# Optimization experiments

Measured on AMD Instinct MI355X. Metric: run time of the kernel, lower is better.

Reference implementation:

```python
import jax, jax.numpy as jnp
import numpy as np

# Dimensions
N = 12288      # fact nodes (batched graph)
B = 64         # examples in batch
R = 36         # image regions per example (hardcoded .repeat(36,1) in source)
E = 196608     # fact-graph edges (avg degree 16)
D_IN = 512     # in_dims
D_OUT = 512    # out_dims
P = 256        # img_att_proj_dim
D_IMG = 1024   # img_dim


def setup_inputs() -> dict:
    key = jax.random.key(0)
    ks = jax.random.split(key, 12)

    def w(k, shape, fan_in):
        return jax.random.normal(k, shape, dtype=jnp.float32) / np.float32(np.sqrt(fan_in))

    return {
        "h": jax.random.normal(ks[0], (N, D_IN), dtype=jnp.float32),
        "img_feats": jax.random.normal(ks[1], (B, R, D_IMG), dtype=jnp.float32),
        "batch_ids": jax.random.randint(ks[2], (N,), 0, B, dtype=jnp.int32),
        "src": jax.random.randint(ks[3], (E,), 0, N, dtype=jnp.int32),
        "dst": jax.random.randint(ks[4], (E,), 0, N, dtype=jnp.int32),
        # cross_att_fact_proj
        "Wf": w(ks[5], (D_IN, P), D_IN), "bf": jnp.zeros((P,), jnp.float32),
        # cross_att_img_proj
        "Wi": w(ks[6], (D_IMG, P), D_IMG), "bi": jnp.zeros((P,), jnp.float32),
        # att_proj (P -> 1)
        "Wa": w(ks[7], (P, 1), P), "ba": jnp.zeros((1,), jnp.float32),
        # node_fc
        "Wn": w(ks[8], (D_IN, D_OUT), D_IN), "bn": jnp.zeros((D_OUT,), jnp.float32),
        # img_fc
        "Wim": w(ks[9], (D_IMG, D_OUT), D_IMG), "bim": jnp.zeros((D_OUT,), jnp.float32),
        # apply_fc (2*out -> out)
        "Wap": w(ks[10], (2 * D_OUT, D_OUT), 2 * D_OUT), "bap": jnp.zeros((D_OUT,), jnp.float32),
    }


def reference(h, img_feats, batch_ids, src, dst,
              Wf, bf, Wi, bi, Wa, ba, Wn, bn, Wim, bim, Wap, bap):
    # ---- apply_node: cross-modal attention over the node's 36 image regions ----
    node_proj = h @ Wf + bf                                   # [N, P]
    img_proj = img_feats @ Wi + bi                            # [B, R, P]
    img_proj_n = img_proj[batch_ids]                          # [N, R, P] gather per node's example
    logits = (jnp.tanh(node_proj[:, None, :] + img_proj_n) @ Wa)[..., 0] + ba[0]  # [N, R]
    att = jax.nn.softmax(logits, axis=1)                      # softmax over 36 regions
    img_n = img_feats[batch_ids]                              # [N, R, D_IMG]
    img = jnp.einsum("nr,nrd->nd", att, img_n)               # [N, D_IMG] attended image feature
    h1 = h @ Wn + bn                                          # node_fc updates 'h' [N, D_OUT]

    # ---- update_all: copy_src('h') messages, sum reduce over in-neighbors ----
    neigh = jax.ops.segment_sum(h1[src], dst, num_segments=N)  # [N, D_OUT]
    msg = neigh + img @ Wim + bim                              # [N, D_OUT]

    # ---- reduce: concat + apply_fc + relu ----
    out = jax.nn.relu(jnp.concatenate([msg, h1], axis=1) @ Wap + bap)  # [N, D_OUT]
    return out
```

## Files before the change

### kernel.cpp

```cpp
#include <hip/hip_runtime.h>
#include <cstdint>
#include <cstddef>

#define N_NODES 12288
#define B_EX    64
#define R_REG   36
#define E_EDGES 196608
#define DD_IN   512
#define DD_OUT  512
#define P_DIM   256
#define D_IMG   1024
#define TANH_C  2.885390081777927f

#define A2_LD     1024
#define NEIGH_OFF 0
#define H1_OFF    512

typedef unsigned short ushort;
typedef __bf16 bf16x8 __attribute__((ext_vector_type(8)));
typedef float f32x4 __attribute__((ext_vector_type(4)));
typedef ushort ushort4v __attribute__((ext_vector_type(4)));
typedef ushort ushort8v __attribute__((ext_vector_type(8)));

__device__ __forceinline__ ushort f2bf(float f) {
    uint32_t u = __float_as_uint(f);
    uint32_t r = (u + 0x7fffu + ((u >> 16) & 1u)) >> 16;
    return (ushort)r;
}
__device__ __forceinline__ float bf2f(ushort u) {
    return __uint_as_float(((uint32_t)u) << 16);
}
__device__ __forceinline__ void gload_lds16(const void* g, void* l) {
    __builtin_amdgcn_global_load_lds((const __attribute__((address_space(1))) void*)g,
                                     (__attribute__((address_space(3))) void*)l, 16, 0, 0);
}
__device__ __forceinline__ void stage_f32(const float* __restrict__ src, void* ldsDst) {
    float4 v0 = *(const float4*)src;
    float4 v1 = *(const float4*)(src + 4);
    ushort8v o;
    o[0] = f2bf(v0.x); o[1] = f2bf(v0.y); o[2] = f2bf(v0.z); o[3] = f2bf(v0.w);
    o[4] = f2bf(v1.x); o[5] = f2bf(v1.y); o[6] = f2bf(v1.z); o[7] = f2bf(v1.w);
    *(ushort8v*)ldsDst = o;
}
__device__ __forceinline__ float fexp2(float x) {
    float r; asm("v_exp_f32 %0, %1" : "=v"(r) : "v"(x)); return r;
}
__device__ __forceinline__ float frcp(float x) {
    float r; asm("v_rcp_f32 %0, %1" : "=v"(r) : "v"(x)); return r;
}
__device__ __forceinline__ int xcd_swz(int lin, int nwg) {
    if ((nwg & 7) == 0) return (lin & 7) * (nwg >> 3) + (lin >> 3);
    return lin;
}

#define PCVT_BLKS (N_NODES * DD_IN / 4 / 256)
#define TR_BLKS   352
#define ZERO_INTS (2 * N_NODES + 2 * B_EX)
#define ZERO_BLKS ((ZERO_INTS + 255) / 256)
__global__ __launch_bounds__(256) void preamble(
    const float* __restrict__ h, ushort* __restrict__ h_bf,
    const float* __restrict__ Wf, const float* __restrict__ Wn,
    const float* __restrict__ Wi, const float* __restrict__ Wap,
    ushort* __restrict__ WfnT, ushort* __restrict__ WiZT,
    ushort* __restrict__ Wap1T, ushort* __restrict__ BT2,
    int* __restrict__ zero_p)
{
    if (blockIdx.x < PCVT_BLKS) {
        int i = blockIdx.x * 256 + threadIdx.x;
        float4 v = ((const float4*)h)[i];
        ushort4v o;
        o[0] = f2bf(v.x); o[1] = f2bf(v.y); o[2] = f2bf(v.z); o[3] = f2bf(v.w);
        ((ushort4v*)h_bf)[i] = o;
        return;
    }
    if (blockIdx.x >= PCVT_BLKS + TR_BLKS) {
        int i = (blockIdx.x - PCVT_BLKS - TR_BLKS) * 256 + threadIdx.x;
        if (i < ZERO_INTS) zero_p[i] = 0;
        return;
    }
    int t = blockIdx.x - PCVT_BLKS;
    const float* W; ushort* WT; int N, ldt, gx;
    if (t < 32)       { W = Wf;  WT = WfnT;                        N = 256; ldt = 512;  gx = 4; }
    else if (t < 96)  { W = Wn;  WT = WfnT + 256 * 512;            N = 512; ldt = 512;  gx = 8; t -= 32; }
    else if (t < 160) { W = Wi;  WT = WiZT;                        N = 256; ldt = 1024; gx = 4; t -= 96; }
    else if (t < 224) { W = Wap; WT = Wap1T;                       N = 512; ldt = 512;  gx = 8; t -= 160; }
    else if (t < 288) { W = Wap; WT = BT2 + NEIGH_OFF;             N = 512; ldt = 1024; gx = 8; t -= 224; }
    else              { W = Wap + 512 * 512; WT = BT2 + H1_OFF;    N = 512; ldt = 1024; gx = 8; t -= 288; }
    const int n0 = (t % gx) * 64, k0 = (t / gx) * 64;

    __shared__ float tt[64][65];
    const int tx = threadIdx.x & 15, ty = threadIdx.x >> 4;
#pragma unroll
    for (int r = 0; r < 4; ++r) {
        float4 v = *(const float4*)&W[(size_t)(k0 + ty * 4 + r) * N + n0 + tx * 4];
        tt[ty * 4 + r][tx * 4 + 0] = v.x;
        tt[ty * 4 + r][tx * 4 + 1] = v.y;
        tt[ty * 4 + r][tx * 4 + 2] = v.z;
        tt[ty * 4 + r][tx * 4 + 3] = v.w;
    }
    __syncthreads();
    const int nl = threadIdx.x >> 2, kq = (threadIdx.x & 3) * 16;
    ushort u[16] __attribute__((aligned(16)));
#pragma unroll
    for (int c = 0; c < 16; ++c) u[c] = f2bf(tt[kq + c][nl]);
    ushort* d = &WT[(size_t)(n0 + nl) * ldt + k0 + kq];
    *(ushort8v*)d = *(ushort8v*)&u[0];
    *(ushort8v*)(d + 8) = *(ushort8v*)&u[8];
}

#define CNT_BLKS (E_EDGES / 256 + N_NODES / 256)
__global__ __launch_bounds__(256) void k2_count_wp(
    const int* __restrict__ dst, const int* __restrict__ bid,
    int* __restrict__ deg, int* __restrict__ bcnt,
    const ushort* __restrict__ Wap1T, const float* __restrict__ Wim,
    ushort* __restrict__ WiZT)
{
    __shared__ ushort As[128 * 64];
    __shared__ ushort Bs[128 * 64];
    if (blockIdx.x < CNT_BLKS) {
        int b = blockIdx.x;
        if (b < E_EDGES / 256) {
            atomicAdd(&deg[dst[b * 256 + threadIdx.x]], 1);
        } else {
            atomicAdd(&bcnt[bid[(b - E_EDGES / 256) * 256 + threadIdx.x]], 1);
        }
        return;
    }
    const int K = DD_IN;
    const int tid = threadIdx.x;
    const int lane = tid & 63;
    const int wid = tid >> 6;
    const int wm = wid >> 1, wn = wid & 1;
    const int lin = blockIdx.x - CNT_BLKS;
    const int m0 = (lin >> 3) * 128, n0 = (lin & 7) * 128;

    f32x4 acc[4][4] = {};
    const int srow = tid >> 3;
    const int schk = tid & 7;
    const char* AsB = (const char*)As;
    const char* BsB = (const char*)Bs;

    for (int k0 = 0; k0 < K; k0 += 64) {
#pragma unroll
        for (int i = 0; i < 4; ++i) {
            int row = i * 32 + srow;
            int ca = (schk ^ (row & 7)) * 8;
            gload_lds16(Wap1T + (size_t)(m0 + row) * K + k0 + ca,
                        (char*)As + i * 4096 + wid * 1024);
            stage_f32(Wim + (size_t)(n0 + row) * K + k0 + ca,
                      (char*)Bs + i * 4096 + wid * 1024 + lane * 16);
        }
        __syncthreads();
#pragma unroll
        for (int kk = 0; kk < 2; ++kk) {
            const int kc = kk * 4 + (lane >> 4);
            bf16x8 af[4], bfr[4];
#pragma unroll
            for (int i = 0; i < 4; ++i) {
                int row = wm * 64 + i * 16 + (lane & 15);
                af[i] = *(const bf16x8*)(AsB + row * 128 + ((kc ^ (row & 7)) << 4));
            }
#pragma unroll
            for (int j = 0; j < 4; ++j) {
                int col = wn * 64 + j * 16 + (lane & 15);
                bfr[j] = *(const bf16x8*)(BsB + col * 128 + ((kc ^ (col & 7)) << 4));
            }
#pragma unroll
            for (int i = 0; i < 4; ++i)
#pragma unroll
                for (int j = 0; j < 4; ++j)
                    acc[i][j] = __builtin_amdgcn_mfma_f32_16x16x32_bf16(af[i], bfr[j], acc[i][j], 0, 0, 0);
        }
        __syncthreads();
    }

#pragma unroll
    for (int i = 0; i < 4; ++i)
#pragma unroll
        for (int j = 0; j < 4; ++j)
#pragma unroll
            for (int q = 0; q < 4; ++q) {
                int row = m0 + wm * 64 + i * 16 + (lane >> 4) * 4 + q;
                int col = n0 + wn * 64 + j * 16 + (lane & 15);
                WiZT[(size_t)(256 + row) * D_IMG + col] = f2bf(acc[i][j][q]);
            }
}

__global__ __launch_bounds__(256) void k3_scan_imgz(
    const int* __restrict__ deg, int* __restrict__ offs,
    const int* __restrict__ bcnt, int* __restrict__ boffs,
    const float* __restrict__ bim, const float* __restrict__ Wap,
    const float* __restrict__ bap, float* __restrict__ bp,
    const float* __restrict__ imgf, const ushort* __restrict__ WiZT,
    const float* __restrict__ bi, float* __restrict__ img_proj,
    ushort* __restrict__ Z)
{
    __shared__ ushort As[128 * 64];
    __shared__ ushort Bs[128 * 64];
    const int t = threadIdx.x;
    if (blockIdx.x < 4) {
        if (blockIdx.x == 0) {
            __shared__ int s[257];
            const int base = t * 48;
            int sum = 0;
            for (int j = 0; j < 48; ++j) sum += deg[base + j];
            s[t] = sum;
            __syncthreads();
            if (t == 0) {
                int acc = 0;
                for (int i = 0; i < 256; ++i) { int v = s[i]; s[i] = acc; acc += v; }
                s[256] = acc;
            }
            __syncthreads();
            int run = s[t];
            for (int j = 0; j < 48; ++j) { offs[base + j] = run; run += deg[base + j]; }
            if (t == 255) offs[N_NODES] = s[256];
        } else if (blockIdx.x == 1) {
            if (t == 0) {
                int acc = 0;
                for (int i = 0; i < B_EX; ++i) { boffs[i] = acc; acc += bcnt[i]; }
                boffs[B_EX] = acc;
            }
        } else {
            int n = (blockIdx.x - 2) * 256 + t;
            float s = bap[n];
            for (int k = 0; k < DD_OUT; ++k) s += bim[k] * Wap[(size_t)k * DD_OUT + n];
            bp[n] = s;
        }
        return;
    }
    const int K = D_IMG;
    const int lane = t & 63;
    const int wid = t >> 6;
    const int wm = wid >> 1, wn = wid & 1;
    const int lin = blockIdx.x - 4;
    const int m0 = (lin / 6) * 128, n0 = (lin % 6) * 128;

    f32x4 acc[4][4] = {};
    const int srow = t >> 3;
    const int schk = t & 7;
    const char* AsB = (const char*)As;
    const char* BsB = (const char*)Bs;

    for (int k0 = 0; k0 < K; k0 += 64) {
#pragma unroll
        for (int i = 0; i < 4; ++i) {
            int row = i * 32 + srow;
            int ca = (schk ^ (row & 7)) * 8;
            stage_f32(imgf + (size_t)(m0 + row) * K + k0 + ca,
                      (char*)As + i * 4096 + wid * 1024 + lane * 16);
            gload_lds16(WiZT + (size_t)(n0 + row) * K + k0 + ca,
                        (char*)Bs + i * 4096 + wid * 1024);
        }
        __syncthreads();
#pragma unroll
        for (int kk = 0; kk < 2; ++kk) {
            const int kc = kk * 4 + (lane >> 4);
            bf16x8 af[4], bfr[4];
#pragma unroll
            for (int i = 0; i < 4; ++i) {
                int row = wm * 64 + i * 16 + (lane & 15);
                af[i] = *(const bf16x8*)(AsB + row * 128 + ((kc ^ (row & 7)) << 4));
            }
#pragma unroll
            for (int j = 0; j < 4; ++j) {
                int col = wn * 64 + j * 16 + (lane & 15);
                bfr[j] = *(const bf16x8*)(BsB + col * 128 + ((kc ^ (col & 7)) << 4));
            }
#pragma unroll
            for (int i = 0; i < 4; ++i)
#pragma unroll
                for (int j = 0; j < 4; ++j)
                    acc[i][j] = __builtin_amdgcn_mfma_f32_16x16x32_bf16(af[i], bfr[j], acc[i][j], 0, 0, 0);
        }
        __syncthreads();
    }

    if (n0 < 256) {
#pragma unroll
        for (int i = 0; i < 4; ++i)
#pragma unroll
            for (int j = 0; j < 4; ++j)
#pragma unroll
                for (int q = 0; q < 4; ++q) {
                    int row = m0 + wm * 64 + i * 16 + (lane >> 4) * 4 + q;
                    int col = n0 + wn * 64 + j * 16 + (lane & 15);
                    img_proj[(size_t)row * P_DIM + col] = acc[i][j][q] + bi[col];
                }
    } else {
#pragma unroll
        for (int i = 0; i < 4; ++i)
#pragma unroll
            for (int j = 0; j < 4; ++j)
#pragma unroll
                for (int q = 0; q < 4; ++q) {
                    int row = m0 + wm * 64 + i * 16 + (lane >> 4) * 4 + q;
                    int col = n0 - 256 + wn * 64 + j * 16 + (lane & 15);
                    Z[(size_t)row * DD_OUT + col] = f2bf(acc[i][j][q]);
                }
    }
}

__global__ __launch_bounds__(256) void k4_scatter_ff(
    const int* __restrict__ src, const int* __restrict__ dst,
    const int* __restrict__ offs, int* __restrict__ cur, int* __restrict__ ssrc,
    const int* __restrict__ bid, const int* __restrict__ boffs,
    int* __restrict__ bcur, int* __restrict__ nlist,
    const ushort* __restrict__ h_bf, const ushort* __restrict__ WfnT,
    const float* __restrict__ biasF, const float* __restrict__ biasN,
    float* __restrict__ node_proj_s, ushort* __restrict__ A2)
{
    __shared__ ushort As[128 * 64];
    __shared__ ushort Bs[64 * 64];
    if (blockIdx.x < CNT_BLKS) {
        int b = blockIdx.x;
        if (b < E_EDGES / 256) {
            int i = b * 256 + threadIdx.x;
            int d = dst[i];
            int p = offs[d] + atomicAdd(&cur[d], 1);
            ssrc[p] = src[i];
        } else {
            int i = (b - E_EDGES / 256) * 256 + threadIdx.x;
            int e = bid[i];
            int p = boffs[e] + atomicAdd(&bcur[e], 1);
            nlist[p] = i;
        }
        return;
    }
    const int K = DD_IN;
    const int tid = threadIdx.x;
    const int lane = tid & 63;
    const int wid = tid >> 6;
    const int lin = xcd_swz(blockIdx.x - CNT_BLKS, 1152);
    const int m0 = (lin / 12) * 128, n0 = (lin % 12) * 64;

    f32x4 acc[2][4] = {};
    const int srow = tid >> 3;
    const int schk = tid & 7;
    const char* AsB = (const char*)As;
    const char* BsB = (const char*)Bs;

    for (int k0 = 0; k0 < K; k0 += 64) {
#pragma unroll
        for (int i = 0; i < 4; ++i) {
            int row = i * 32 + srow;
            int ca = (schk ^ (row & 7)) * 8;
            gload_lds16(h_bf + (size_t)(m0 + row) * K + k0 + ca,
                        (char*)As + i * 4096 + wid * 1024);
        }
#pragma unroll
        for (int i = 0; i < 2; ++i) {
            int row = i * 32 + srow;
            int cb = (schk ^ (row & 7)) * 8;
            gload_lds16(WfnT + (size_t)(n0 + row) * K + k0 + cb,
                        (char*)Bs + i * 4096 + wid * 1024);
        }
        __syncthreads();
#pragma unroll
        for (int kk = 0; kk < 2; ++kk) {
            const int kc = kk * 4 + (lane >> 4);
            bf16x8 af[2], bfr[4];
#pragma unroll
            for (int i = 0; i < 2; ++i) {
                int row = wid * 32 + i * 16 + (lane & 15);
                af[i] = *(const bf16x8*)(AsB + row * 128 + ((kc ^ (row & 7)) << 4));
            }
#pragma unroll
            for (int j = 0; j < 4; ++j) {
                int col = j * 16 + (lane & 15);
                bfr[j] = *(const bf16x8*)(BsB + col * 128 + ((kc ^ (col & 7)) << 4));
            }
#pragma unroll
            for (int i = 0; i < 2; ++i)
#pragma unroll
                for (int j = 0; j < 4; ++j)
                    acc[i][j] = __builtin_amdgcn_mfma_f32_16x16x32_bf16(af[i], bfr[j], acc[i][j], 0, 0, 0);
        }
        __syncthreads();
    }

    if (n0 < 256) {
#pragma unroll
        for (int i = 0; i < 2; ++i)
#pragma unroll
            for (int j = 0; j < 4; ++j)
#pragma unroll
                for (int q = 0; q < 4; ++q) {
                    int row = m0 + wid * 32 + i * 16 + (lane >> 4) * 4 + q;
                    int col = n0 + j * 16 + (lane & 15);
                    node_proj_s[(size_t)row * P_DIM + col] = (acc[i][j][q] + biasF[col]) * TANH_C;
                }
    } else {
#pragma unroll
        for (int i = 0; i < 2; ++i)
#pragma unroll
            for (int j = 0; j < 4; ++j)
#pragma unroll
                for (int q = 0; q < 4; ++q) {
                    int row = m0 + wid * 32 + i * 16 + (lane >> 4) * 4 + q;
                    int col = n0 - 256 + j * 16 + (lane & 15);
                    A2[(size_t)row * A2_LD + H1_OFF + col] = f2bf(acc[i][j][q] + biasN[col]);
                }
    }
}

__device__ __forceinline__ void acc8(float* a, uint4 v) {
    a[0] += bf2f((ushort)(v.x & 0xffffu)); a[1] += bf2f((ushort)(v.x >> 16));
    a[2] += bf2f((ushort)(v.y & 0xffffu)); a[3] += bf2f((ushort)(v.y >> 16));
    a[4] += bf2f((ushort)(v.z & 0xffffu)); a[5] += bf2f((ushort)(v.z >> 16));
    a[6] += bf2f((ushort)(v.w & 0xffffu)); a[7] += bf2f((ushort)(v.w >> 16));
}

__global__ __launch_bounds__(256) void k5_att_gather(
    const float* __restrict__ node_proj_s, const float* __restrict__ img_proj,
    const int* __restrict__ batch_ids, const float* __restrict__ Wa,
    const ushort* __restrict__ Z, ushort* __restrict__ imgz,
    const int* __restrict__ off, const int* __restrict__ ssrc,
    const ushort* __restrict__ A2h1, ushort* __restrict__ A2nb)
{
    __shared__ float red[4][R_REG][20];
    const int lane = threadIdx.x & 63;
    const int wv = threadIdx.x >> 6;
    if (blockIdx.x < N_NODES / 4) {
        const int n = blockIdx.x * 4 + wv;
        const int b = batch_ids[n];

        const float4 nps = *(const float4*)(node_proj_s + (size_t)n * P_DIM + 4 * lane);
        const float4 wa = *(const float4*)(Wa + 4 * lane);
        const float* ip0 = img_proj + (size_t)b * R_REG * P_DIM + 4 * lane;

#pragma unroll
        for (int r = 0; r < R_REG; ++r) {
            float4 ip = *(const float4*)(ip0 + (size_t)r * P_DIM);
            float t0 = fexp2(fmaf(ip.x, TANH_C, nps.x));
            float t1 = fexp2(fmaf(ip.y, TANH_C, nps.y));
            float t2 = fexp2(fmaf(ip.z, TANH_C, nps.z));
            float t3 = fexp2(fmaf(ip.w, TANH_C, nps.w));
            float p;
            p = wa.x * frcp(t0 + 1.f);
            p = fmaf(wa.y, frcp(t1 + 1.f), p);
            p = fmaf(wa.z, frcp(t2 + 1.f), p);
            p = fmaf(wa.w, frcp(t3 + 1.f), p);
            p += __shfl_xor(p, 16);
            p += __shfl_xor(p, 32);
            if (lane < 16) red[wv][r][lane] = p;
        }
        __syncthreads();

        float logit = -INFINITY;
        if (lane < R_REG) {
            const float* row = &red[wv][lane][0];
            float4 a = *(const float4*)row;
            float4 bq = *(const float4*)(row + 4);
            float4 c = *(const float4*)(row + 8);
            float4 d = *(const float4*)(row + 12);
            float s01 = ((a.x + a.y) + (a.z + a.w)) + ((bq.x + bq.y) + (bq.z + bq.w));
            float s23 = ((c.x + c.y) + (c.z + c.w)) + ((d.x + d.y) + (d.z + d.w));
            logit = -2.f * (s01 + s23);
        }
        float m = logit;
#pragma unroll
        for (int o = 32; o; o >>= 1) m = fmaxf(m, __shfl_xor(m, o));
        float e = (lane < R_REG) ? __expf(logit - m) : 0.f;
        float s = e;
#pragma unroll
        for (int o = 32; o; o >>= 1) s += __shfl_xor(s, o);
        float inv_s = frcp(s);
        if (lane < R_REG) red[wv][lane][16] = e * inv_s;

        float az[8] = {};
        const ushort* zb = Z + (size_t)b * R_REG * DD_OUT + lane * 8;
#pragma unroll 4
        for (int r = 0; r < R_REG; ++r) {
            uint4 zv = *(const uint4*)(zb + (size_t)r * DD_OUT);
            float a = red[wv][r][16];
            az[0] = fmaf(a, bf2f((ushort)(zv.x & 0xffffu)), az[0]);
            az[1] = fmaf(a, bf2f((ushort)(zv.x >> 16)),     az[1]);
            az[2] = fmaf(a, bf2f((ushort)(zv.y & 0xffffu)), az[2]);
            az[3] = fmaf(a, bf2f((ushort)(zv.y >> 16)),     az[3]);
            az[4] = fmaf(a, bf2f((ushort)(zv.z & 0xffffu)), az[4]);
            az[5] = fmaf(a, bf2f((ushort)(zv.z >> 16)),     az[5]);
            az[6] = fmaf(a, bf2f((ushort)(zv.w & 0xffffu)), az[6]);
            az[7] = fmaf(a, bf2f((ushort)(zv.w >> 16)),     az[7]);
        }
        ushort8v zo;
#pragma unroll
        for (int i = 0; i < 8; ++i) zo[i] = f2bf(az[i]);
        *(ushort8v*)(imgz + (size_t)n * DD_OUT + lane * 8) = zo;
        return;
    }
    const int n = (blockIdx.x - N_NODES / 4) * 4 + wv;
    const int e0 = off[n], e1 = off[n + 1];

    float a[8] = {};
    int e = e0;
    for (; e + 4 <= e1; e += 4) {
        int s0 = ssrc[e], s1 = ssrc[e + 1], s2 = ssrc[e + 2], s3 = ssrc[e + 3];
        uint4 v0 = *(const uint4*)(A2h1 + (size_t)s0 * A2_LD + lane * 8);
        uint4 v1 = *(const uint4*)(A2h1 + (size_t)s1 * A2_LD + lane * 8);
        uint4 v2 = *(const uint4*)(A2h1 + (size_t)s2 * A2_LD + lane * 8);
        uint4 v3 = *(const uint4*)(A2h1 + (size_t)s3 * A2_LD + lane * 8);
        acc8(a, v0); acc8(a, v1); acc8(a, v2); acc8(a, v3);
    }
    for (; e < e1; ++e) {
        int s0 = ssrc[e];
        uint4 v0 = *(const uint4*)(A2h1 + (size_t)s0 * A2_LD + lane * 8);
        acc8(a, v0);
    }
    ushort8v o;
#pragma unroll
    for (int i = 0; i < 8; ++i) o[i] = f2bf(a[i]);
    *(ushort8v*)(A2nb + (size_t)n * A2_LD + lane * 8) = o;
}

__global__ __launch_bounds__(256) void gemm_out(
    const ushort* __restrict__ A, const ushort* __restrict__ BT,
    const float* __restrict__ bias, const ushort* __restrict__ Cadd,
    float* __restrict__ Cf)
{
    __shared__ ushort As[128 * 64];
    __shared__ ushort Bs[64 * 64];
    const int K = A2_LD;
    const int tid = threadIdx.x;
    const int lane = tid & 63;
    const int wid = tid >> 6;
    const int lin = xcd_swz(blockIdx.y * 8 + blockIdx.x, 768);
    const int m0 = (lin >> 3) * 128, n0 = (lin & 7) * 64;

    f32x4 acc[2][4] = {};
    const int srow = tid >> 3;
    const int schk = tid & 7;
    const char* AsB = (const char*)As;
    const char* BsB = (const char*)Bs;

    for (int k0 = 0; k0 < K; k0 += 64) {
#pragma unroll
        for (int i = 0; i < 4; ++i) {
            int row = i * 32 + srow;
            int ca = (schk ^ (row & 7)) * 8;
            gload_lds16(A + (size_t)(m0 + row) * K + k0 + ca,
                        (char*)As + i * 4096 + wid * 1024);
        }
#pragma unroll
        for (int i = 0; i < 2; ++i) {
            int row = i * 32 + srow;
            int cb = (schk ^ (row & 7)) * 8;
            gload_lds16(BT + (size_t)(n0 + row) * K + k0 + cb,
                        (char*)Bs + i * 4096 + wid * 1024);
        }
        __syncthreads();
#pragma unroll
        for (int kk = 0; kk < 2; ++kk) {
            const int kc = kk * 4 + (lane >> 4);
            bf16x8 af[2], bfr[4];
#pragma unroll
            for (int i = 0; i < 2; ++i) {
                int row = wid * 32 + i * 16 + (lane & 15);
                af[i] = *(const bf16x8*)(AsB + row * 128 + ((kc ^ (row & 7)) << 4));
            }
#pragma unroll
            for (int j = 0; j < 4; ++j) {
                int col = j * 16 + (lane & 15);
                bfr[j] = *(const bf16x8*)(BsB + col * 128 + ((kc ^ (col & 7)) << 4));
            }
#pragma unroll
            for (int i = 0; i < 2; ++i)
#pragma unroll
                for (int j = 0; j < 4; ++j)
                    acc[i][j] = __builtin_amdgcn_mfma_f32_16x16x32_bf16(af[i], bfr[j], acc[i][j], 0, 0, 0);
        }
        __syncthreads();
    }

#pragma unroll
    for (int i = 0; i < 2; ++i)
#pragma unroll
        for (int j = 0; j < 4; ++j)
#pragma unroll
            for (int q = 0; q < 4; ++q) {
                int row = m0 + wid * 32 + i * 16 + (lane >> 4) * 4 + q;
                int col = n0 + j * 16 + (lane & 15);
                float v = acc[i][j][q] + bias[col] + bf2f(Cadd[(size_t)row * DD_OUT + col]);
                Cf[(size_t)row * DD_OUT + col] = fmaxf(v, 0.f);
            }
}

extern "C" void kernel_launch(void* const* d_in, const int* in_sizes, int n_in,
                              void* d_out, int out_size, void* d_ws, size_t ws_size,
                              hipStream_t stream) {
    const float* h         = (const float*)d_in[0];
    const float* img_feats = (const float*)d_in[1];
    const int*   batch_ids = (const int*)d_in[2];
    const int*   src       = (const int*)d_in[3];
    const int*   dst       = (const int*)d_in[4];
    const float* Wf  = (const float*)d_in[5];
    const float* bf  = (const float*)d_in[6];
    const float* Wi  = (const float*)d_in[7];
    const float* bi  = (const float*)d_in[8];
    const float* Wa  = (const float*)d_in[9];
    const float* Wn  = (const float*)d_in[11];
    const float* bn  = (const float*)d_in[12];
    const float* Wim = (const float*)d_in[13];
    const float* bim = (const float*)d_in[14];
    const float* Wap = (const float*)d_in[15];
    const float* bap = (const float*)d_in[16];
    float* out = (float*)d_out;
    float* ws  = (float*)d_ws;

    ushort* A2      = (ushort*)(ws + 0);
    ushort* imgz    = (ushort*)(ws + 6291456);
    float*  node_proj = ws + 12582912;
    float*  img_proj  = ws + 15728640;
    ushort* Z      = (ushort*)(ws + 16760832);
    ushort* h_bf   = (ushort*)(ws + 17350656);
    ushort* WfnT   = (ushort*)(ws + 20496384);
    ushort* WiZT   = (ushort*)(ws + 20692992);
    ushort* Wap1T  = (ushort*)(ws + 21086208);
    ushort* BT2    = (ushort*)(ws + 21217280);
    float*  bprime = ws + 21479424;
    int* deg  = (int*)(ws + 21479936);
    int* cur  = deg + N_NODES;
    int* bcnt = cur + N_NODES;
    int* bcur = bcnt + B_EX;
    int* offs = bcur + B_EX;
    int* boffs = offs + N_NODES + 1;
    int* ssrc = boffs + B_EX + 1;
    int* nlist = ssrc + E_EDGES;

    dim3 blk(256);

    preamble<<<dim3(PCVT_BLKS + TR_BLKS + ZERO_BLKS), blk, 0, stream>>>(
        h, h_bf, Wf, Wn, Wi, Wap, WfnT, WiZT, Wap1T, BT2, deg);
    k2_count_wp<<<dim3(CNT_BLKS + 32), blk, 0, stream>>>(
        dst, batch_ids, deg, bcnt, Wap1T, Wim, WiZT);
    k3_scan_imgz<<<dim3(4 + 108), blk, 0, stream>>>(
        deg, offs, bcnt, boffs, bim, Wap, bap, bprime,
        img_feats, WiZT, bi, img_proj, Z);
    k4_scatter_ff<<<dim3(CNT_BLKS + 1152), blk, 0, stream>>>(
        src, dst, offs, cur, ssrc, batch_ids, boffs, bcur, nlist,
        h_bf, WfnT, bf, bn, node_proj, A2);
    k5_att_gather<<<dim3(2 * (N_NODES / 4)), blk, 0, stream>>>(
        node_proj, img_proj, batch_ids, Wa, Z, imgz,
        offs, ssrc, A2 + H1_OFF, A2 + NEIGH_OFF);
    gemm_out<<<dim3(8, 96), blk, 0, stream>>>(A2, BT2, bprime, imgz, out);
}
```

Measured before the change: 209.9 us.

## Re-partition kernel stages: merge node-feature GEMM with imgZ GEMM, batch-sort in one block

Moves the per-example node counting and sort into a single block of the count kernel, which uses shared-memory atomics and removes the bcnt/boffs global arrays. The node_fc/fact-projection GEMM moves into the same launch as the image projection GEMM. The attention computation now runs alongside the edge scatter, iterating nodes in batch-sorted order so that nodes sharing an example's image data run close together. The goal is better overlap between stages and cache reuse of img_proj and Z. The trade-off is a serial single-block sort of 12288 nodes and a different load balance across the merged kernels.

```diff
diff --git a/kernel.cpp b/kernel.cpp
--- a/kernel.cpp
+++ b/kernel.cpp
@@ -55,8 +55,8 @@
 
 #define PCVT_BLKS (N_NODES * DD_IN / 4 / 256)
 #define TR_BLKS   352
-#define ZERO_INTS (2 * N_NODES + 2 * B_EX)
-#define ZERO_BLKS ((ZERO_INTS + 255) / 256)
+#define ZERO_INTS (2 * N_NODES)
+#define ZERO_BLKS (ZERO_INTS / 256)
 __global__ __launch_bounds__(256) void preamble(
     const float* __restrict__ h, ushort* __restrict__ h_bf,
     const float* __restrict__ Wf, const float* __restrict__ Wn,
@@ -108,21 +108,38 @@
     *(ushort8v*)(d + 8) = *(ushort8v*)&u[8];
 }
 
-#define CNT_BLKS (E_EDGES / 256 + N_NODES / 256)
-__global__ __launch_bounds__(256) void k2_count_wp(
+#define ECNT_BLKS (E_EDGES / 256)
+__global__ __launch_bounds__(256) void k2_count_sort_wp(
     const int* __restrict__ dst, const int* __restrict__ bid,
-    int* __restrict__ deg, int* __restrict__ bcnt,
+    int* __restrict__ deg, int* __restrict__ nlist,
     const ushort* __restrict__ Wap1T, const float* __restrict__ Wim,
     ushort* __restrict__ WiZT)
 {
     __shared__ ushort As[128 * 64];
     __shared__ ushort Bs[128 * 64];
-    if (blockIdx.x < CNT_BLKS) {
-        int b = blockIdx.x;
-        if (b < E_EDGES / 256) {
-            atomicAdd(&deg[dst[b * 256 + threadIdx.x]], 1);
-        } else {
-            atomicAdd(&bcnt[bid[(b - E_EDGES / 256) * 256 + threadIdx.x]], 1);
+    if (blockIdx.x < ECNT_BLKS) {
+        atomicAdd(&deg[dst[blockIdx.x * 256 + threadIdx.x]], 1);
+        return;
+    }
+    if (blockIdx.x == ECNT_BLKS) {
+        __shared__ int bc[B_EX];
+        __shared__ int bo[B_EX];
+        if (threadIdx.x < B_EX) bc[threadIdx.x] = 0;
+        __syncthreads();
+        for (int i = threadIdx.x; i < N_NODES; i += 256)
+            atomicAdd(&bc[bid[i]], 1);
+        __syncthreads();
+        if (threadIdx.x == 0) {
+            int acc = 0;
+            for (int i = 0; i < B_EX; ++i) { bo[i] = acc; acc += bc[i]; }
+        }
+        __syncthreads();
+        if (threadIdx.x < B_EX) bc[threadIdx.x] = 0;
+        __syncthreads();
+        for (int i = threadIdx.x; i < N_NODES; i += 256) {
+            int b = bid[i];
+            int p = bo[b] + atomicAdd(&bc[b], 1);
+            nlist[p] = i;
         }
         return;
     }
@@ -131,7 +148,7 @@
     const int lane = tid & 63;
     const int wid = tid >> 6;
     const int wm = wid >> 1, wn = wid & 1;
-    const int lin = blockIdx.x - CNT_BLKS;
+    const int lin = blockIdx.x - (ECNT_BLKS + 1);
     const int m0 = (lin >> 3) * 128, n0 = (lin & 7) * 128;
 
     f32x4 acc[4][4] = {};
@@ -186,19 +203,23 @@
             }
 }
 
-__global__ __launch_bounds__(256) void k3_scan_imgz(
+#define IMGZ_BASE 3
+#define FF_BASE   111
+__global__ __launch_bounds__(256) void k3_scan_imgz_ff(
     const int* __restrict__ deg, int* __restrict__ offs,
-    const int* __restrict__ bcnt, int* __restrict__ boffs,
     const float* __restrict__ bim, const float* __restrict__ Wap,
     const float* __restrict__ bap, float* __restrict__ bp,
     const float* __restrict__ imgf, const ushort* __restrict__ WiZT,
     const float* __restrict__ bi, float* __restrict__ img_proj,
-    ushort* __restrict__ Z)
+    ushort* __restrict__ Z,
+    const ushort* __restrict__ h_bf, const ushort* __restrict__ WfnT,
+    const float* __restrict__ biasF, const float* __restrict__ biasN,
+    float* __restrict__ node_proj_s, ushort* __restrict__ A2)
 {
     __shared__ ushort As[128 * 64];
     __shared__ ushort Bs[128 * 64];
     const int t = threadIdx.x;
-    if (blockIdx.x < 4) {
+    if (blockIdx.x < IMGZ_BASE) {
         if (blockIdx.x == 0) {
             __shared__ int s[257];
             const int base = t * 48;
@@ -215,128 +236,94 @@
             int run = s[t];
             for (int j = 0; j < 48; ++j) { offs[base + j] = run; run += deg[base + j]; }
             if (t == 255) offs[N_NODES] = s[256];
-        } else if (blockIdx.x == 1) {
-            if (t == 0) {
-                int acc = 0;
-                for (int i = 0; i < B_EX; ++i) { boffs[i] = acc; acc += bcnt[i]; }
-                boffs[B_EX] = acc;
-            }
         } else {
-            int n = (blockIdx.x - 2) * 256 + t;
+            int n = (blockIdx.x - 1) * 256 + t;
             float s = bap[n];
             for (int k = 0; k < DD_OUT; ++k) s += bim[k] * Wap[(size_t)k * DD_OUT + n];
             bp[n] = s;
         }
         return;
     }
-    const int K = D_IMG;
     const int lane = t & 63;
     const int wid = t >> 6;
-    const int wm = wid >> 1, wn = wid & 1;
-    const int lin = blockIdx.x - 4;
-    const int m0 = (lin / 6) * 128, n0 = (lin % 6) * 128;
-
-    f32x4 acc[4][4] = {};
+    if (blockIdx.x < FF_BASE) {
+        const int K = D_IMG;
+        const int wm = wid >> 1, wn = wid & 1;
+        const int lin = blockIdx.x - IMGZ_BASE;
+        const int m0 = (lin / 6) * 128, n0 = (lin % 6) * 128;
+
+        f32x4 acc[4][4] = {};
+        const int srow = t >> 3;
+        const int schk = t & 7;
+        const char* AsB = (const char*)As;
+        const char* BsB = (const char*)Bs;
+
+        for (int k0 = 0; k0 < K; k0 += 64) {
+#pragma unroll
+            for (int i = 0; i < 4; ++i) {
+                int row = i * 32 + srow;
+                int ca = (schk ^ (row & 7)) * 8;
+                stage_f32(imgf + (size_t)(m0 + row) * K + k0 + ca,
+                          (char*)As + i * 4096 + wid * 1024 + lane * 16);
+                gload_lds16(WiZT + (size_t)(n0 + row) * K + k0 + ca,
+                            (char*)Bs + i * 4096 + wid * 1024);
+            }
+            __syncthreads();
+#pragma unroll
+            for (int kk = 0; kk < 2; ++kk) {
+                const int kc = kk * 4 + (lane >> 4);
+                bf16x8 af[4], bfr[4];
+#pragma unroll
+                for (int i = 0; i < 4; ++i) {
+                    int row = wm * 64 + i * 16 + (lane & 15);
+                    af[i] = *(const bf16x8*)(AsB + row * 128 + ((kc ^ (row & 7)) << 4));
+                }
+#pragma unroll
+                for (int j = 0; j < 4; ++j) {
+                    int col = wn * 64 + j * 16 + (lane & 15);
+                    bfr[j] = *(const bf16x8*)(BsB + col * 128 + ((kc ^ (col & 7)) << 4));
+                }
+#pragma unroll
+                for (int i = 0; i < 4; ++i)
+#pragma unroll
+                    for (int j = 0; j < 4; ++j)
+                        acc[i][j] = __builtin_amdgcn_mfma_f32_16x16x32_bf16(af[i], bfr[j], acc[i][j], 0, 0, 0);
+            }
+            __syncthreads();
+        }
+
+        if (n0 < 256) {
+#pragma unroll
+            for (int i = 0; i < 4; ++i)
+#pragma unroll
+                for (int j = 0; j < 4; ++j)
+#pragma unroll
+                    for (int q = 0; q < 4; ++q) {
+                        int row = m0 + wm * 64 + i * 16 + (lane >> 4) * 4 + q;
+                        int col = n0 + wn * 64 + j * 16 + (lane & 15);
+                        img_proj[(size_t)row * P_DIM + col] = acc[i][j][q] + bi[col];
+                    }
+        } else {
+#pragma unroll
+            for (int i = 0; i < 4; ++i)
+#pragma unroll
+                for (int j = 0; j < 4; ++j)
+#pragma unroll
+                    for (int q = 0; q < 4; ++q) {
+                        int row = m0 + wm * 64 + i * 16 + (lane >> 4) * 4 + q;
+                        int col = n0 - 256 + wn * 64 + j * 16 + (lane & 15);
+                        Z[(size_t)row * DD_OUT + col] = f2bf(acc[i][j][q]);
+                    }
+        }
+        return;
+    }
+    const int K = DD_IN;
+    const int lin = xcd_swz(blockIdx.x - FF_BASE, 1152);
+    const int m0 = (lin / 12) * 128, n0 = (lin % 12) * 64;
+
+    f32x4 acc[2][4] = {};
     const int srow = t >> 3;
     const int schk = t & 7;
-    const char* AsB = (const char*)As;
-    const char* BsB = (const char*)Bs;
-
-    for (int k0 = 0; k0 < K; k0 += 64) {
-#pragma unroll
-        for (int i = 0; i < 4; ++i) {
-            int row = i * 32 + srow;
-            int ca = (schk ^ (row & 7)) * 8;
-            stage_f32(imgf + (size_t)(m0 + row) * K + k0 + ca,
-                      (char*)As + i * 4096 + wid * 1024 + lane * 16);
-            gload_lds16(WiZT + (size_t)(n0 + row) * K + k0 + ca,
-                        (char*)Bs + i * 4096 + wid * 1024);
-        }
-        __syncthreads();
-#pragma unroll
-        for (int kk = 0; kk < 2; ++kk) {
-            const int kc = kk * 4 + (lane >> 4);
-            bf16x8 af[4], bfr[4];
-#pragma unroll
-            for (int i = 0; i < 4; ++i) {
-                int row = wm * 64 + i * 16 + (lane & 15);
-                af[i] = *(const bf16x8*)(AsB + row * 128 + ((kc ^ (row & 7)) << 4));
-            }
-#pragma unroll
-            for (int j = 0; j < 4; ++j) {
-                int col = wn * 64 + j * 16 + (lane & 15);
-                bfr[j] = *(const bf16x8*)(BsB + col * 128 + ((kc ^ (col & 7)) << 4));
-            }
-#pragma unroll
-            for (int i = 0; i < 4; ++i)
-#pragma unroll
-                for (int j = 0; j < 4; ++j)
-                    acc[i][j] = __builtin_amdgcn_mfma_f32_16x16x32_bf16(af[i], bfr[j], acc[i][j], 0, 0, 0);
-        }
-        __syncthreads();
-    }
-
-    if (n0 < 256) {
-#pragma unroll
-        for (int i = 0; i < 4; ++i)
-#pragma unroll
-            for (int j = 0; j < 4; ++j)
-#pragma unroll
-                for (int q = 0; q < 4; ++q) {
-                    int row = m0 + wm * 64 + i * 16 + (lane >> 4) * 4 + q;
-                    int col = n0 + wn * 64 + j * 16 + (lane & 15);
-                    img_proj[(size_t)row * P_DIM + col] = acc[i][j][q] + bi[col];
-                }
-    } else {
-#pragma unroll
-        for (int i = 0; i < 4; ++i)
-#pragma unroll
-            for (int j = 0; j < 4; ++j)
-#pragma unroll
-                for (int q = 0; q < 4; ++q) {
-                    int row = m0 + wm * 64 + i * 16 + (lane >> 4) * 4 + q;
-                    int col = n0 - 256 + wn * 64 + j * 16 + (lane & 15);
-                    Z[(size_t)row * DD_OUT + col] = f2bf(acc[i][j][q]);
-                }
-    }
-}
-
-__global__ __launch_bounds__(256) void k4_scatter_ff(
-    const int* __restrict__ src, const int* __restrict__ dst,
-    const int* __restrict__ offs, int* __restrict__ cur, int* __restrict__ ssrc,
-    const int* __restrict__ bid, const int* __restrict__ boffs,
-    int* __restrict__ bcur, int* __restrict__ nlist,
-    const ushort* __restrict__ h_bf, const ushort* __restrict__ WfnT,
-    const float* __restrict__ biasF, const float* __restrict__ biasN,
-    float* __restrict__ node_proj_s, ushort* __restrict__ A2)
-{
-    __shared__ ushort As[128 * 64];
-    __shared__ ushort Bs[64 * 64];
-    if (blockIdx.x < CNT_BLKS) {
-        int b = blockIdx.x;
-        if (b < E_EDGES / 256) {
-            int i = b * 256 + threadIdx.x;
-            int d = dst[i];
-            int p = offs[d] + atomicAdd(&cur[d], 1);
-            ssrc[p] = src[i];
-        } else {
-            int i = (b - E_EDGES / 256) * 256 + threadIdx.x;
-            int e = bid[i];
-            int p = boffs[e] + atomicAdd(&bcur[e], 1);
-            nlist[p] = i;
-        }
-        return;
-    }
-    const int K = DD_IN;
-    const int tid = threadIdx.x;
-    const int lane = tid & 63;
-    const int wid = tid >> 6;
-    const int lin = xcd_swz(blockIdx.x - CNT_BLKS, 1152);
-    const int m0 = (lin / 12) * 128, n0 = (lin % 12) * 64;
-
-    f32x4 acc[2][4] = {};
-    const int srow = tid >> 3;
-    const int schk = tid & 7;
     const char* AsB = (const char*)As;
     const char* BsB = (const char*)Bs;
 
@@ -404,6 +391,91 @@
     }
 }
 
+__global__ __launch_bounds__(256) void k4_scatter_att(
+    const int* __restrict__ src, const int* __restrict__ dst,
+    const int* __restrict__ offs, int* __restrict__ cur, int* __restrict__ ssrc,
+    const float* __restrict__ node_proj_s, const float* __restrict__ img_proj,
+    const int* __restrict__ batch_ids, const float* __restrict__ Wa,
+    const ushort* __restrict__ Z, ushort* __restrict__ imgz,
+    const int* __restrict__ nlist)
+{
+    __shared__ float red[4][R_REG][20];
+    if (blockIdx.x < ECNT_BLKS) {
+        int i = blockIdx.x * 256 + threadIdx.x;
+        int d = dst[i];
+        int p = offs[d] + atomicAdd(&cur[d], 1);
+        ssrc[p] = src[i];
+        return;
+    }
+    const int lane = threadIdx.x & 63;
+    const int wv = threadIdx.x >> 6;
+    const int n = nlist[(blockIdx.x - ECNT_BLKS) * 4 + wv];
+    const int b = batch_ids[n];
+
+    const float4 nps = *(const float4*)(node_proj_s + (size_t)n * P_DIM + 4 * lane);
+    const float4 wa = *(const float4*)(Wa + 4 * lane);
+    const float* ip0 = img_proj + (size_t)b * R_REG * P_DIM + 4 * lane;
+
+#pragma unroll
+    for (int r = 0; r < R_REG; ++r) {
+        float4 ip = *(const float4*)(ip0 + (size_t)r * P_DIM);
+        float t0 = fexp2(fmaf(ip.x, TANH_C, nps.x));
+        float t1 = fexp2(fmaf(ip.y, TANH_C, nps.y));
+        float t2 = fexp2(fmaf(ip.z, TANH_C, nps.z));
+        float t3 = fexp2(fmaf(ip.w, TANH_C, nps.w));
+        float p;
+        p = wa.x * frcp(t0 + 1.f);
+        p = fmaf(wa.y, frcp(t1 + 1.f), p);
+        p = fmaf(wa.z, frcp(t2 + 1.f), p);
+        p = fmaf(wa.w, frcp(t3 + 1.f), p);
+        p += __shfl_xor(p, 16);
+        p += __shfl_xor(p, 32);
+        if (lane < 16) red[wv][r][lane] = p;
+    }
+    __syncthreads();
+
+    float logit = -INFINITY;
+    if (lane < R_REG) {
+        const float* row = &red[wv][lane][0];
+        float4 a = *(const float4*)row;
+        float4 bq = *(const float4*)(row + 4);
+        float4 c = *(const float4*)(row + 8);
+        float4 d = *(const float4*)(row + 12);
+        float s01 = ((a.x + a.y) + (a.z + a.w)) + ((bq.x + bq.y) + (bq.z + bq.w));
+        float s23 = ((c.x + c.y) + (c.z + c.w)) + ((d.x + d.y) + (d.z + d.w));
+        logit = -2.f * (s01 + s23);
+    }
+    float m = logit;
+#pragma unroll
+    for (int o = 32; o; o >>= 1) m = fmaxf(m, __shfl_xor(m, o));
+    float e = (lane < R_REG) ? __expf(logit - m) : 0.f;
+    float s = e;
+#pragma unroll
+    for (int o = 32; o; o >>= 1) s += __shfl_xor(s, o);
+    float inv_s = frcp(s);
+    if (lane < R_REG) red[wv][lane][16] = e * inv_s;
+
+    float az[8] = {};
+    const ushort* zb = Z + (size_t)b * R_REG * DD_OUT + lane * 8;
+#pragma unroll 4
+    for (int r = 0; r < R_REG; ++r) {
+        uint4 zv = *(const uint4*)(zb + (size_t)r * DD_OUT);
+        float a = red[wv][r][16];
+        az[0] = fmaf(a, bf2f((ushort)(zv.x & 0xffffu)), az[0]);
+        az[1] = fmaf(a, bf2f((ushort)(zv.x >> 16)),     az[1]);
+        az[2] = fmaf(a, bf2f((ushort)(zv.y & 0xffffu)), az[2]);
+        az[3] = fmaf(a, bf2f((ushort)(zv.y >> 16)),     az[3]);
+        az[4] = fmaf(a, bf2f((ushort)(zv.z & 0xffffu)), az[4]);
+        az[5] = fmaf(a, bf2f((ushort)(zv.z >> 16)),     az[5]);
+        az[6] = fmaf(a, bf2f((ushort)(zv.w & 0xffffu)), az[6]);
+        az[7] = fmaf(a, bf2f((ushort)(zv.w >> 16)),     az[7]);
+    }
+    ushort8v zo;
+#pragma unroll
+    for (int i = 0; i < 8; ++i) zo[i] = f2bf(az[i]);
+    *(ushort8v*)(imgz + (size_t)n * DD_OUT + lane * 8) = zo;
+}
+
 __device__ __forceinline__ void acc8(float* a, uint4 v) {
     a[0] += bf2f((ushort)(v.x & 0xffffu)); a[1] += bf2f((ushort)(v.x >> 16));
     a[2] += bf2f((ushort)(v.y & 0xffffu)); a[3] += bf2f((ushort)(v.y >> 16));
@@ -411,85 +483,13 @@
     a[6] += bf2f((ushort)(v.w & 0xffffu)); a[7] += bf2f((ushort)(v.w >> 16));
 }
 
-__global__ __launch_bounds__(256) void k5_att_gather(
-    const float* __restrict__ node_proj_s, const float* __restrict__ img_proj,
-    const int* __restrict__ batch_ids, const float* __restrict__ Wa,
-    const ushort* __restrict__ Z, ushort* __restrict__ imgz,
+__global__ __launch_bounds__(256) void k5_gather(
     const int* __restrict__ off, const int* __restrict__ ssrc,
     const ushort* __restrict__ A2h1, ushort* __restrict__ A2nb)
 {
-    __shared__ float red[4][R_REG][20];
     const int lane = threadIdx.x & 63;
     const int wv = threadIdx.x >> 6;
-    if (blockIdx.x < N_NODES / 4) {
-        const int n = blockIdx.x * 4 + wv;
-        const int b = batch_ids[n];
-
-        const float4 nps = *(const float4*)(node_proj_s + (size_t)n * P_DIM + 4 * lane);
-        const float4 wa = *(const float4*)(Wa + 4 * lane);
-        const float* ip0 = img_proj + (size_t)b * R_REG * P_DIM + 4 * lane;
-
-#pragma unroll
-        for (int r = 0; r < R_REG; ++r) {
-            float4 ip = *(const float4*)(ip0 + (size_t)r * P_DIM);
-            float t0 = fexp2(fmaf(ip.x, TANH_C, nps.x));
-            float t1 = fexp2(fmaf(ip.y, TANH_C, nps.y));
-            float t2 = fexp2(fmaf(ip.z, TANH_C, nps.z));
-            float t3 = fexp2(fmaf(ip.w, TANH_C, nps.w));
-            float p;
-            p = wa.x * frcp(t0 + 1.f);
-            p = fmaf(wa.y, frcp(t1 + 1.f), p);
-            p = fmaf(wa.z, frcp(t2 + 1.f), p);
-            p = fmaf(wa.w, frcp(t3 + 1.f), p);
-            p += __shfl_xor(p, 16);
-            p += __shfl_xor(p, 32);
-            if (lane < 16) red[wv][r][lane] = p;
-        }
-        __syncthreads();
-
-        float logit = -INFINITY;
-        if (lane < R_REG) {
-            const float* row = &red[wv][lane][0];
-            float4 a = *(const float4*)row;
-            float4 bq = *(const float4*)(row + 4);
-            float4 c = *(const float4*)(row + 8);
-            float4 d = *(const float4*)(row + 12);
-            float s01 = ((a.x + a.y) + (a.z + a.w)) + ((bq.x + bq.y) + (bq.z + bq.w));
-            float s23 = ((c.x + c.y) + (c.z + c.w)) + ((d.x + d.y) + (d.z + d.w));
-            logit = -2.f * (s01 + s23);
-        }
-        float m = logit;
-#pragma unroll
-        for (int o = 32; o; o >>= 1) m = fmaxf(m, __shfl_xor(m, o));
-        float e = (lane < R_REG) ? __expf(logit - m) : 0.f;
-        float s = e;
-#pragma unroll
-        for (int o = 32; o; o >>= 1) s += __shfl_xor(s, o);
-        float inv_s = frcp(s);
-        if (lane < R_REG) red[wv][lane][16] = e * inv_s;
-
-        float az[8] = {};
-        const ushort* zb = Z + (size_t)b * R_REG * DD_OUT + lane * 8;
-#pragma unroll 4
-        for (int r = 0; r < R_REG; ++r) {
-            uint4 zv = *(const uint4*)(zb + (size_t)r * DD_OUT);
-            float a = red[wv][r][16];
-            az[0] = fmaf(a, bf2f((ushort)(zv.x & 0xffffu)), az[0]);
-            az[1] = fmaf(a, bf2f((ushort)(zv.x >> 16)),     az[1]);
-            az[2] = fmaf(a, bf2f((ushort)(zv.y & 0xffffu)), az[2]);
-            az[3] = fmaf(a, bf2f((ushort)(zv.y >> 16)),     az[3]);
-            az[4] = fmaf(a, bf2f((ushort)(zv.z & 0xffffu)), az[4]);
-            az[5] = fmaf(a, bf2f((ushort)(zv.z >> 16)),     az[5]);
-            az[6] = fmaf(a, bf2f((ushort)(zv.w & 0xffffu)), az[6]);
-            az[7] = fmaf(a, bf2f((ushort)(zv.w >> 16)),     az[7]);
-        }
-        ushort8v zo;
-#pragma unroll
-        for (int i = 0; i < 8; ++i) zo[i] = f2bf(az[i]);
-        *(ushort8v*)(imgz + (size_t)n * DD_OUT + lane * 8) = zo;
-        return;
-    }
-    const int n = (blockIdx.x - N_NODES / 4) * 4 + wv;
+    const int n = blockIdx.x * 4 + wv;
     const int e0 = off[n], e1 = off[n + 1];
 
     float a[8] = {};
@@ -620,27 +620,24 @@
     float*  bprime = ws + 21479424;
     int* deg  = (int*)(ws + 21479936);
     int* cur  = deg + N_NODES;
-    int* bcnt = cur + N_NODES;
-    int* bcur = bcnt + B_EX;
-    int* offs = bcur + B_EX;
-    int* boffs = offs + N_NODES + 1;
-    int* ssrc = boffs + B_EX + 1;
+    int* offs = cur + N_NODES;
+    int* ssrc = offs + N_NODES + 1;
     int* nlist = ssrc + E_EDGES;
 
     dim3 blk(256);
 
     preamble<<<dim3(PCVT_BLKS + TR_BLKS + ZERO_BLKS), blk, 0, stream>>>(
         h, h_bf, Wf, Wn, Wi, Wap, WfnT, WiZT, Wap1T, BT2, deg);
-    k2_count_wp<<<dim3(CNT_BLKS + 32), blk, 0, stream>>>(
-        dst, batch_ids, deg, bcnt, Wap1T, Wim, WiZT);
-    k3_scan_imgz<<<dim3(4 + 108), blk, 0, stream>>>(
-        deg, offs, bcnt, boffs, bim, Wap, bap, bprime,
-        img_feats, WiZT, bi, img_proj, Z);
-    k4_scatter_ff<<<dim3(CNT_BLKS + 1152), blk, 0, stream>>>(
-        src, dst, offs, cur, ssrc, batch_ids, boffs, bcur, nlist,
+    k2_count_sort_wp<<<dim3(ECNT_BLKS + 1 + 32), blk, 0, stream>>>(
+        dst, batch_ids, deg, nlist, Wap1T, Wim, WiZT);
+    k3_scan_imgz_ff<<<dim3(FF_BASE + 1152), blk, 0, stream>>>(
+        deg, offs, bim, Wap, bap, bprime,
+        img_feats, WiZT, bi, img_proj, Z,
         h_bf, WfnT, bf, bn, node_proj, A2);
-    k5_att_gather<<<dim3(2 * (N_NODES / 4)), blk, 0, stream>>>(
-        node_proj, img_proj, batch_ids, Wa, Z, imgz,
+    k4_scatter_att<<<dim3(ECNT_BLKS + N_NODES / 4), blk, 0, stream>>>(
+        src, dst, offs, cur, ssrc,
+        node_proj, img_proj, batch_ids, Wa, Z, imgz, nlist);
+    k5_gather<<<dim3(N_NODES / 4), blk, 0, stream>>>(
         offs, ssrc, A2 + H1_OFF, A2 + NEIGH_OFF);
     gemm_out<<<dim3(8, 96), blk, 0, stream>>>(A2, BT2, bprime, imgz, out);
 }
```

Measured after the change: 187.1 us. 10.9% less time.
